# Optimization experiments

Hardware: AMD Instinct MI355X
Metric: run time of the kernel (lower is better)

Reference implementation:

```python
import jax, jax.numpy as jnp
import numpy as np

H = 256
NUM_REL = 480
NUM_ENT = 23000
N_TRIPLES = 8192
T = 10  # cur_ts == path_len window


def _lin_params(key, din, dout):
    kw, _ = jax.random.split(key)
    W = jax.random.normal(kw, (din, dout), dtype=jnp.float32) * 0.02
    b = jnp.zeros((dout,), dtype=jnp.float32)
    return W, b


def setup_inputs() -> dict:
    key = jax.random.key(0)
    ks = jax.random.split(key, 16)
    pre_emb = jax.random.normal(ks[0], (NUM_ENT, H), dtype=jnp.float32)
    r_emb = jax.random.normal(ks[1], (NUM_REL, H), dtype=jnp.float32)
    # history counts: sparse non-negative (zeros are masked to -1e9 in softmax)
    part = jax.random.uniform(ks[2], (N_TRIPLES, T * NUM_REL), dtype=jnp.float32)
    mask = jax.random.uniform(ks[3], (N_TRIPLES, T * NUM_REL)) < 0.3
    partial_embeding = jnp.where(mask, part, 0.0)
    sub_idx = jax.random.randint(ks[4], (N_TRIPLES,), 0, NUM_ENT)
    rel_idx = jax.random.randint(ks[5], (N_TRIPLES,), 0, NUM_REL)
    obj_idx = jax.random.randint(ks[6], (N_TRIPLES,), 0, NUM_ENT)
    Wm1, bm1 = _lin_params(ks[7], H, 2 * H)
    Wm2, bm2 = _lin_params(ks[8], 2 * H, H)
    Wattn, battn = _lin_params(ks[9], H, H)
    Wh1, bh1 = _lin_params(ks[10], H, H)
    Wh2, bh2 = _lin_params(ks[11], H, H)
    Walign, balign = _lin_params(ks[12], H, H)
    Wih = jax.random.normal(ks[13], (H, 3 * H), dtype=jnp.float32) * 0.02
    Whh = jax.random.normal(ks[14], (H, 3 * H), dtype=jnp.float32) * 0.02
    bih = jnp.zeros((3 * H,), dtype=jnp.float32)
    bhh = jnp.zeros((3 * H,), dtype=jnp.float32)
    return dict(pre_emb=pre_emb, r_emb=r_emb, partial_embeding=partial_embeding,
                sub_idx=sub_idx, rel_idx=rel_idx, obj_idx=obj_idx, cur_ts=T,
                Wm1=Wm1, bm1=bm1, Wm2=Wm2, bm2=bm2, Wattn=Wattn, battn=battn,
                Wh1=Wh1, bh1=bh1, Wh2=Wh2, bh2=bh2, Walign=Walign, balign=balign,
                Wih=Wih, Whh=Whh, bih=bih, bhh=bhh)


def _gru_cell(x, h, Wih, Whh, bih, bhh):
    # torch.nn.GRUCell math
    gi = x @ Wih + bih
    gh = h @ Whh + bhh
    i_r, i_z, i_n = jnp.split(gi, 3, axis=-1)
    h_r, h_z, h_n = jnp.split(gh, 3, axis=-1)
    r = jax.nn.sigmoid(i_r + h_r)
    z = jax.nn.sigmoid(i_z + h_z)
    n = jnp.tanh(i_n + r * h_n)
    return (1.0 - z) * n + z * h


def reference(pre_emb, r_emb, partial_embeding, sub_idx, rel_idx, obj_idx, cur_ts,
              Wm1, bm1, Wm2, bm2, Wattn, battn, Wh1, bh1, Wh2, bh2,
              Walign, balign, Wih, Whh, bih, bhh):
    n = partial_embeding.shape[0]
    num_rel = r_emb.shape[0]
    t = cur_ts  # path window covers [0, cur_ts)
    # relation mapping
    mapped_rel = (r_emb @ Wm1 + bm1) @ Wm2 + bm2            # [R, H]
    q_rel = mapped_rel[rel_idx]                               # [N, H]
    # attention logits base (loop-invariant): q W_attn mapped_rel^T
    base = (q_rel @ Wattn + battn) @ mapped_rel.T            # [N, R]
    # [N, t*R] -> [t, N, R] time-major slices
    hist = partial_embeding[:, : t * num_rel].reshape(n, t, num_rel).swapaxes(0, 1)
    h0 = jnp.zeros((n, mapped_rel.shape[1]), dtype=pre_emb.dtype)

    def step(h, cur):
        attn = cur * base
        attn = jax.nn.softmax(jnp.where(attn == 0, -1e9, attn), axis=1)
        x = attn @ mapped_rel                                 # [N, H]
        return _gru_cell(x, h, Wih, Whh, bih, bhh), None

    gru_hidden, _ = jax.lax.scan(step, h0, hist)
    # predicted history + match loss
    predicted_hist = 0.1 * ((q_rel @ Wh1 + bh1) @ Wh2 + bh2) + q_rel
    match_loss = jnp.mean((predicted_hist - gru_hidden) ** 2)
    # forward_forth (distmult)
    h2 = _gru_cell(q_rel, predicted_hist, Wih, Whh, bih, bhh)  # [N, H]
    sub = pre_emb[sub_idx]
    score_ = ((sub @ Walign + balign) * h2) @ (pre_emb @ Walign + balign).T  # [N, E]
    # BCE(sigmoid(score_), one_hot(obj)): per-elem -y*logsig(s) - (1-y)*logsig(-s)
    pos = score_[jnp.arange(n), obj_idx]
    path_loss = (-jnp.sum(jax.nn.log_sigmoid(-score_)) - jnp.sum(pos)) / (score_.size)
    score = jax.nn.sigmoid(score_)
    return match_loss, path_loss, score
```

## Files before the change

### kernel.cpp

```cpp
#include <hip/hip_runtime.h>
#include <hip/hip_bf16.h>
#include <stdint.h>

#define DEV __device__ __forceinline__

typedef unsigned short u16;
typedef __attribute__((ext_vector_type(8))) short bf16x8;
typedef __attribute__((ext_vector_type(4))) float f32x4;
typedef __attribute__((ext_vector_type(4))) unsigned short u16x4;

constexpr int H  = 256;
constexpr int R  = 480;
constexpr int RP = 512;
constexpr int NE = 23000;
constexpr int NT = 8192;
constexpr int TT = 10;

DEV u16 f2b(float f) {
  union { float f; unsigned u; } x; x.f = f;
  unsigned u = x.u;
  return (u16)((u + 0x7fffu + ((u >> 16) & 1u)) >> 16);
}
DEV float b2f(u16 h) {
  union { unsigned u; float f; } x; x.u = ((unsigned)h) << 16;
  return x.f;
}

DEV void gload_lds16(const u16* g, u16* lds) {
  __builtin_amdgcn_global_load_lds(
      (const __attribute__((address_space(1))) unsigned int*)g,
      (__attribute__((address_space(3))) unsigned int*)lds, 16, 0, 0);
}

__launch_bounds__(256)
__global__ void stageA_k(const float* __restrict__ r_emb,
                         const float* __restrict__ Wm1, const float* __restrict__ bm1,
                         const float* __restrict__ Wm2, const float* __restrict__ bm2,
                         const float* __restrict__ Wattn, const float* __restrict__ battn,
                         const float* __restrict__ Wih,
                         const float* __restrict__ Wh1, const float* __restrict__ bh1,
                         const float* __restrict__ Wh2, const float* __restrict__ bh2,
                         const float* __restrict__ Whh, const float* __restrict__ bhh,
                         const float* __restrict__ bih,
                         float* __restrict__ mapped, float* __restrict__ t1,
                         float* __restrict__ Pg, float* __restrict__ G2,
                         u16* __restrict__ MWT) {
  __shared__ float re[256], hid[512], mp[256], p1l[256], Pl[256];
  const int r = blockIdx.x, j = threadIdx.x;
  re[j] = r_emb[(size_t)r * 256 + j];
  __syncthreads();
  float s0 = bm1[j], s1 = bm1[j + 256];
  for (int k = 0; k < 256; ++k) {
    const float a = re[k];
    s0 += a * Wm1[(size_t)k * 512 + j];
    s1 += a * Wm1[(size_t)k * 512 + j + 256];
  }
  hid[j] = s0; hid[j + 256] = s1;
  __syncthreads();
  float m = bm2[j];
  for (int k = 0; k < 512; ++k) m += hid[k] * Wm2[(size_t)k * 256 + j];
  mp[j] = m; mapped[(size_t)r * 256 + j] = m;
  __syncthreads();
  float tv = battn[j];
  for (int k = 0; k < 256; ++k) tv += mp[k] * Wattn[(size_t)k * 256 + j];
  t1[(size_t)r * 256 + j] = tv;
  float mw0 = 0.f, mw1 = 0.f, mw2 = 0.f;
  for (int k = 0; k < 256; ++k) {
    const float a = mp[k];
    mw0 += a * Wih[(size_t)k * 768 + j];
    mw1 += a * Wih[(size_t)k * 768 + j + 256];
    mw2 += a * Wih[(size_t)k * 768 + j + 512];
  }
  MWT[(size_t)j * RP + r] = f2b(mw0);
  MWT[(size_t)(j + 256) * RP + r] = f2b(mw1);
  MWT[(size_t)(j + 512) * RP + r] = f2b(mw2);
  float pv = bh1[j];
  for (int k = 0; k < 256; ++k) pv += mp[k] * Wh1[(size_t)k * 256 + j];
  p1l[j] = pv;
  __syncthreads();
  float Pv = bh2[j];
  for (int k = 0; k < 256; ++k) Pv += p1l[k] * Wh2[(size_t)k * 256 + j];
  Pv = 0.1f * Pv + mp[j];
  Pl[j] = Pv; Pg[(size_t)r * 256 + j] = Pv;
  __syncthreads();
  float pw0 = bhh[j], pw1 = bhh[j + 256], pw2 = bhh[j + 512];
  for (int k = 0; k < 256; ++k) {
    const float a = Pl[k];
    pw0 += a * Whh[(size_t)k * 768 + j];
    pw1 += a * Whh[(size_t)k * 768 + j + 256];
    pw2 += a * Whh[(size_t)k * 768 + j + 512];
  }
  const float rg = 1.f / (1.f + __expf(-(mw0 + bih[j] + pw0)));
  const float zg = 1.f / (1.f + __expf(-(mw1 + bih[j + 256] + pw1)));
  const float ng = tanhf(mw2 + bih[j + 512] + rg * pw2);
  G2[(size_t)r * 256 + j] = (1.f - zg) * ng + zg * Pv;
}

__global__ void sgemm_bt_k(const float* __restrict__ A, const float* __restrict__ W,
                           float* __restrict__ C, int M, int N, int K) {
  const int idx = blockIdx.x * 256 + threadIdx.x;
  if (idx >= M * N) return;
  const int i = idx / N, j = idx % N;
  float s = 0.f;
  const float* a = A + (size_t)i * K;
  const float* w = W + (size_t)j * K;
  for (int k = 0; k < K; ++k) s += a[k] * w[k];
  C[idx] = s;
}

__global__ void prep_k(const float* __restrict__ Whh, const float* __restrict__ Walign,
                       const float* __restrict__ bih, const float* __restrict__ bhh,
                       u16* __restrict__ WhhT, u16* __restrict__ WalignT,
                       float* __restrict__ bsum) {
  const int b = blockIdx.x, tid = threadIdx.x;
  if (b < 768) {
    WhhT[(size_t)b * 256 + tid] = f2b(Whh[(size_t)tid * 768 + b]);
  } else if (b < 1024) {
    const int n = b - 768;
    WalignT[(size_t)n * 256 + tid] = f2b(Walign[(size_t)tid * 256 + n]);
  } else {
    const int c = (b - 1024) * 256 + tid;
    if (c < 768) bsum[c] = bih[c] + (c < 512 ? bhh[c] : 0.f);
  }
}

__global__ void softmax_all_k(const float* __restrict__ part, const float* __restrict__ B480,
                              const int* __restrict__ rel_idx, u16* __restrict__ attn) {
  const int task = blockIdx.x * 4 + (threadIdx.x >> 6);
  const int lane = threadIdx.x & 63;
  const int tt = task >> 13;
  const int i  = task & (NT - 1);
  const float* cur = part + (size_t)i * (TT * R) + (size_t)tt * R;
  const float* b = B480 + (size_t)rel_idx[i] * R;
  float v[8];
  float m = -3e38f;
  #pragma unroll
  for (int j = 0; j < 8; ++j) {
    const int r = lane + j * 64;
    float val = -1e9f;
    if (r < R) {
      const float c = cur[r];
      val = (c == 0.f) ? -1e9f : c * b[r];
      m = fmaxf(m, val);
    }
    v[j] = val;
  }
  #pragma unroll
  for (int o = 32; o; o >>= 1) m = fmaxf(m, __shfl_xor(m, o));
  float s = 0.f;
  #pragma unroll
  for (int j = 0; j < 8; ++j) {
    const int r = lane + j * 64;
    if (r < R) { v[j] = __expf(v[j] - m); s += v[j]; }
  }
  #pragma unroll
  for (int o = 32; o; o >>= 1) s += __shfl_xor(s, o);
  const float inv = 1.f / s;
  u16* arow = attn + (size_t)task * RP;
  #pragma unroll
  for (int j = 0; j < 8; ++j) {
    const int r = lane + j * 64;
    arow[r] = (r < R) ? f2b(v[j] * inv) : (u16)0;
  }
}

__launch_bounds__(256)
__global__ void scan_k(const u16* __restrict__ WhhT, const float* __restrict__ bhh,
                       const u16* __restrict__ gi_all, float* __restrict__ hbuf) {
  __shared__ __align__(16) u16 As[32 * 256];
  __shared__ __align__(16) u16 Bs[2][192 * 64];
  const int tid = threadIdx.x;
  const int lane = tid & 63;
  const int wv = tid >> 6;
  const int rf = wv >> 1;
  const int ch = wv & 1;
  const int fr = lane & 15;
  const int fq = lane >> 4;
  const int row_l = rf * 16 + fr;
  const int grow = blockIdx.x * 32 + row_l;
  const int sw = (fr & 7) * 8;

  auto stageB = [&](int buf, int cg, int k0) {
    #pragma unroll
    for (int it = 0; it < 6; ++it) {
      const int c = it * 256 + tid;
      const int vr = c >> 3, s = c & 7;
      const int vcol = ((vr >> 6) * 256) + cg * 64 + (vr & 63);
      gload_lds16(WhhT + (size_t)vcol * 256 + k0 + ((s ^ (vr & 7)) * 8),
                  &Bs[buf][(it * 256 + wv * 64) * 8]);
    }
  };

  float hreg[4][2][4];
  #pragma unroll
  for (int cg = 0; cg < 4; ++cg)
    #pragma unroll
    for (int nn = 0; nn < 2; ++nn)
      #pragma unroll
      for (int j = 0; j < 4; ++j) hreg[cg][nn][j] = 0.f;

  for (int t = 0; t < TT; ++t) {
    const u16* gi = gi_all + (size_t)t * NT * 768;
    #pragma unroll
    for (int cg = 0; cg < 4; ++cg) {
      f32x4 acc[6] = {};
      u16x4 gv[3][2];
      #pragma unroll
      for (int nn = 0; nn < 2; ++nn) {
        const int c = cg * 64 + ch * 32 + nn * 16 + fq * 4;
        const size_t gb = (size_t)grow * 768 + c;
        gv[0][nn] = *(const u16x4*)&gi[gb];
        gv[1][nn] = *(const u16x4*)&gi[gb + 256];
        gv[2][nn] = *(const u16x4*)&gi[gb + 512];
      }
      if (t > 0) {
        stageB(0, cg, 0);
        #pragma unroll
        for (int ki = 0; ki < 4; ++ki) {
          const int cb = ki & 1;
          if (ki < 3) {
            stageB(cb ^ 1, cg, (ki + 1) * 64);
            asm volatile("s_waitcnt vmcnt(6)" ::: "memory");
          } else {
            asm volatile("s_waitcnt vmcnt(0)" ::: "memory");
          }
          __builtin_amdgcn_sched_barrier(0);
          __builtin_amdgcn_s_barrier();
          #pragma unroll
          for (int kk = 0; kk < 2; ++kk) {
            const int ko = (ki * 64 + kk * 32 + fq * 8) ^ sw;
            const bf16x8 a = *(const bf16x8*)&As[row_l * 256 + ko];
            const int bo = (kk * 32 + fq * 8) ^ sw;
            #pragma unroll
            for (int g = 0; g < 3; ++g)
              #pragma unroll
              for (int nn = 0; nn < 2; ++nn) {
                const int vr = g * 64 + ch * 32 + nn * 16 + fr;
                const bf16x8 b = *(const bf16x8*)&Bs[cb][vr * 64 + bo];
                acc[g * 2 + nn] =
                    __builtin_amdgcn_mfma_f32_16x16x32_bf16(b, a, acc[g * 2 + nn], 0, 0, 0);
              }
          }
          __builtin_amdgcn_s_barrier();
        }
      }
      #pragma unroll
      for (int nn = 0; nn < 2; ++nn) {
        const int c = cg * 64 + ch * 32 + nn * 16 + fq * 4;
        const f32x4 bn = *(const f32x4*)&bhh[512 + c];
        #pragma unroll
        for (int j = 0; j < 4; ++j) {
          const float rg = 1.f / (1.f + __expf(-(b2f(gv[0][nn][j]) + acc[nn][j])));
          const float zg = 1.f / (1.f + __expf(-(b2f(gv[1][nn][j]) + acc[2 + nn][j])));
          const float ng = tanhf(b2f(gv[2][nn][j]) + rg * (acc[4 + nn][j] + bn[j]));
          hreg[cg][nn][j] = (1.f - zg) * ng + zg * hreg[cg][nn][j];
        }
      }
    }
    #pragma unroll
    for (int cg = 0; cg < 4; ++cg)
      #pragma unroll
      for (int nn = 0; nn < 2; ++nn) {
        const int c = cg * 64 + ch * 32 + nn * 16 + fq * 4;
        u16x4 o;
        #pragma unroll
        for (int j = 0; j < 4; ++j) o[j] = f2b(hreg[cg][nn][j]);
        *(u16x4*)&As[row_l * 256 + (c ^ sw)] = o;
        if (t == TT - 1) {
          f32x4 hv;
          #pragma unroll
          for (int j = 0; j < 4; ++j) hv[j] = hreg[cg][nn][j];
          *(f32x4*)&hbuf[(size_t)grow * 256 + c] = hv;
        }
      }
    __syncthreads();
  }
}

__global__ void gather_sub_k(const float* __restrict__ pre, const int* __restrict__ sub,
                             u16* __restrict__ sb) {
  const int q = blockIdx.x * 256 + threadIdx.x;
  const int i = q >> 6, c = (q & 63) * 4;
  const f32x4 v = *(const f32x4*)&pre[(size_t)sub[i] * H + c];
  u16x4 o;
  #pragma unroll
  for (int j = 0; j < 4; ++j) o[j] = f2b(v[j]);
  *(u16x4*)&sb[(size_t)q * 4] = o;
}
__global__ void cvt_pre_k(const float* __restrict__ pre, u16* __restrict__ pb) {
  const int q = blockIdx.x * 256 + threadIdx.x;
  const f32x4 v = *(const f32x4*)&pre[(size_t)q * 4];
  u16x4 o;
  #pragma unroll
  for (int j = 0; j < 4; ++j) o[j] = f2b(v[j]);
  *(u16x4*)&pb[(size_t)q * 4] = o;
}

__global__ void pos_k(const u16* __restrict__ lhs, const u16* __restrict__ alT,
                      const int* __restrict__ obj, float* __restrict__ pos) {
  const int row = blockIdx.x * 4 + (threadIdx.x >> 6);
  const int lane = threadIdx.x & 63;
  const u16x4 av = *(const u16x4*)&lhs[(size_t)row * H + lane * 4];
  const u16x4 bv = *(const u16x4*)&alT[(size_t)obj[row] * H + lane * 4];
  float s = 0.f;
  #pragma unroll
  for (int j = 0; j < 4; ++j) s += b2f(av[j]) * b2f(bv[j]);
  #pragma unroll
  for (int o = 32; o; o >>= 1) s += __shfl_down(s, o);
  if (lane == 0) pos[row] = s;
}

__global__ void finalize_k(const float* __restrict__ mp, const float* __restrict__ sp,
                           const float* __restrict__ pos, float* __restrict__ out) {
  const int tid = threadIdx.x;
  float s1 = 0.f, s2 = 0.f, s3 = 0.f;
  for (int i = tid; i < 128; i += 256) s1 += mp[i];
  for (int i = tid; i < 11520; i += 256) s2 += sp[i];
  for (int i = tid; i < 8192; i += 256) s3 += pos[i];
  #pragma unroll
  for (int o = 32; o; o >>= 1) {
    s1 += __shfl_down(s1, o); s2 += __shfl_down(s2, o); s3 += __shfl_down(s3, o);
  }
  __shared__ float r1[4], r2[4], r3[4];
  if ((tid & 63) == 0) { r1[tid >> 6] = s1; r2[tid >> 6] = s2; r3[tid >> 6] = s3; }
  __syncthreads();
  if (tid == 0) {
    const float a = r1[0] + r1[1] + r1[2] + r1[3];
    const float b = r2[0] + r2[1] + r2[2] + r2[3];
    const float c = r3[0] + r3[1] + r3[2] + r3[3];
    out[0] = a / 2097152.f;
    out[1] = (b - c) / 188416000.f;
  }
}

template <int MODE>
__launch_bounds__(256)
__global__ void gemm_k(const u16* __restrict__ A, const u16* __restrict__ Bt,
                       const float* __restrict__ bias,
                       float* __restrict__ Cf, u16* __restrict__ Cb,
                       int M, int N, int K,
                       float* __restrict__ out2, float* __restrict__ part,
                       const int* __restrict__ rel_idx, const float* __restrict__ Pf,
                       const float* __restrict__ G2f, const float* __restrict__ hf) {
  __shared__ __align__(16) u16 As[128 * 64];
  __shared__ __align__(16) u16 Bs[128 * 64];
  __shared__ float red[4];
  const int tid = threadIdx.x;
  const int lane = tid & 63;
  const int wv = tid >> 6;
  const int nbx = gridDim.x;
  int flat = blockIdx.y * nbx + blockIdx.x;
  const int nwg = nbx * gridDim.y;
  if ((nwg & 7) == 0) flat = (flat & 7) * (nwg >> 3) + (flat >> 3);
  const int bx = flat % nbx;
  const int by = flat / nbx;
  const int m0 = by * 128;
  const int n0 = bx * 128;
  const int wm = (wv >> 1) * 64;
  const int wn = (wv & 1) * 64;
  const int fr = lane & 15;
  const int fq = lane >> 4;
  const int sw = (lane & 7) * 8;
  f32x4 acc[4][4] = {};

  for (int k0 = 0; k0 < K; k0 += 64) {
    __syncthreads();
    #pragma unroll
    for (int it = 0; it < 4; ++it) {
      const int c = it * 256 + tid;
      const int row = c >> 3, s = c & 7;
      const int sc = (s ^ (row & 7)) * 8;
      int gr = m0 + row; gr = gr < M ? gr : M - 1;
      gload_lds16(A + (size_t)gr * K + k0 + sc, &As[(it * 256 + wv * 64) * 8]);
      int nr = n0 + row; nr = nr < N ? nr : N - 1;
      gload_lds16(Bt + (size_t)nr * K + k0 + sc, &Bs[(it * 256 + wv * 64) * 8]);
    }
    __syncthreads();
    #pragma unroll
    for (int kk = 0; kk < 2; ++kk) {
      const int ko = (kk * 32 + fq * 8) ^ sw;
      bf16x8 a[4], b[4];
      #pragma unroll
      for (int mi = 0; mi < 4; ++mi)
        a[mi] = *(const bf16x8*)&As[(wm + mi * 16 + fr) * 64 + ko];
      #pragma unroll
      for (int ni = 0; ni < 4; ++ni)
        b[ni] = *(const bf16x8*)&Bs[(wn + ni * 16 + fr) * 64 + ko];
      #pragma unroll
      for (int mi = 0; mi < 4; ++mi)
        #pragma unroll
        for (int ni = 0; ni < 4; ++ni)
          acc[mi][ni] = __builtin_amdgcn_mfma_f32_16x16x32_bf16(b[ni], a[mi], acc[mi][ni], 0, 0, 0);
    }
  }

  float local = 0.f;
  #pragma unroll
  for (int mi = 0; mi < 4; ++mi) {
    const int rowm = m0 + wm + mi * 16 + fr;
    int rel = 0;
    if (MODE == 2) rel = rel_idx[rowm];
    #pragma unroll
    for (int ni = 0; ni < 4; ++ni) {
      const int col = n0 + wn + ni * 16 + fq * 4;
      if (rowm < M && col < N) {
        f32x4 v = acc[mi][ni];
        if (MODE == 0) {
          if (bias != nullptr) {
            const f32x4 bv = *(const f32x4*)&bias[col];
            #pragma unroll
            for (int j = 0; j < 4; ++j) v[j] += bv[j];
          }
          if (Cf) *(f32x4*)&Cf[(size_t)rowm * N + col] = v;
          if (Cb) {
            u16x4 o;
            #pragma unroll
            for (int j = 0; j < 4; ++j) o[j] = f2b(v[j]);
            *(u16x4*)&Cb[(size_t)rowm * N + col] = o;
          }
        } else if (MODE == 1) {
          f32x4 sg;
          #pragma unroll
          for (int j = 0; j < 4; ++j) {
            const float s = v[j];
            const float sig = 1.f / (1.f + __expf(-s));
            sg[j] = sig;
            const float om = 1.f - sig;
            local += (om > 0.f) ? -__logf(om) : s;
          }
          *(f32x4*)&out2[(size_t)rowm * N + col] = sg;
        } else {
          const f32x4 bv = *(const f32x4*)&bias[col];
          const f32x4 Pv = *(const f32x4*)&Pf[(size_t)rel * H + col];
          const f32x4 Gv = *(const f32x4*)&G2f[(size_t)rel * H + col];
          const f32x4 hv = *(const f32x4*)&hf[(size_t)rowm * H + col];
          u16x4 o;
          #pragma unroll
          for (int j = 0; j < 4; ++j) {
            const float d = Pv[j] - hv[j];
            local += d * d;
            o[j] = f2b((v[j] + bv[j]) * Gv[j]);
          }
          *(u16x4*)&Cb[(size_t)rowm * N + col] = o;
        }
      }
    }
  }
  if (MODE != 0) {
    #pragma unroll
    for (int o = 32; o; o >>= 1) local += __shfl_down(local, o);
    if (lane == 0) red[wv] = local;
    __syncthreads();
    if (tid == 0) part[blockIdx.y * gridDim.x + blockIdx.x] = red[0] + red[1] + red[2] + red[3];
  }
}

extern "C" void kernel_launch(void* const* d_in, const int* in_sizes, int n_in,
                              void* d_out, int out_size, void* d_ws, size_t ws_size,
                              hipStream_t stream) {
  const float* pre_emb = (const float*)d_in[0];
  const float* r_emb   = (const float*)d_in[1];
  const float* part_e  = (const float*)d_in[2];
  const int*   sub_idx = (const int*)d_in[3];
  const int*   rel_idx = (const int*)d_in[4];
  const int*   obj_idx = (const int*)d_in[5];
  const float* Wm1 = (const float*)d_in[7];  const float* bm1 = (const float*)d_in[8];
  const float* Wm2 = (const float*)d_in[9];  const float* bm2 = (const float*)d_in[10];
  const float* Wattn = (const float*)d_in[11]; const float* battn = (const float*)d_in[12];
  const float* Wh1 = (const float*)d_in[13]; const float* bh1 = (const float*)d_in[14];
  const float* Wh2 = (const float*)d_in[15]; const float* bh2 = (const float*)d_in[16];
  const float* Walign = (const float*)d_in[17]; const float* balign = (const float*)d_in[18];
  const float* Wih = (const float*)d_in[19]; const float* Whh = (const float*)d_in[20];
  const float* bih = (const float*)d_in[21]; const float* bhh = (const float*)d_in[22];
  float* out = (float*)d_out;

  char* w = (char*)d_ws;
  size_t off = 0;
  auto alloc = [&](size_t bytes) -> void* {
    off = (off + 255) & ~(size_t)255;
    void* p = w + off;
    off += bytes;
    return p;
  };
  float* mapped = (float*)alloc((size_t)R * H * 4);
  float* t1     = (float*)alloc((size_t)R * H * 4);
  float* B480   = (float*)alloc((size_t)R * R * 4);
  float* P      = (float*)alloc((size_t)R * H * 4);
  float* G2     = (float*)alloc((size_t)R * H * 4);
  u16* MWT      = (u16*)alloc((size_t)768 * RP * 2);
  u16* WhhT     = (u16*)alloc((size_t)768 * H * 2);
  u16* WalignT  = (u16*)alloc((size_t)H * H * 2);
  float* bsum   = (float*)alloc(768 * 4);
  float* hbuf   = (float*)alloc((size_t)NT * H * 4);
  u16* lhs_b    = (u16*)alloc((size_t)NT * H * 2);
  u16* sub_b    = (u16*)alloc((size_t)NT * H * 2);
  u16* pre_b    = (u16*)alloc((size_t)NE * H * 2);
  u16* alT      = (u16*)alloc((size_t)NE * H * 2);
  float* mpart  = (float*)alloc(128 * 4);
  float* spart  = (float*)alloc(11520 * 4);
  float* posar  = (float*)alloc(8192 * 4);
  u16* attn_all = (u16*)alloc((size_t)TT * NT * RP * 2);
  u16* gi_all   = (u16*)alloc((size_t)TT * NT * 768 * 2);
  if (off > ws_size) return;

  hipMemsetAsync(MWT, 0, (size_t)768 * RP * 2, stream);
  stageA_k<<<R, 256, 0, stream>>>(r_emb, Wm1, bm1, Wm2, bm2, Wattn, battn, Wih,
                                  Wh1, bh1, Wh2, bh2, Whh, bhh, bih,
                                  mapped, t1, P, G2, MWT);
  sgemm_bt_k<<<(R * R + 255) / 256, 256, 0, stream>>>(t1, mapped, B480, R, R, H);
  prep_k<<<1027, 256, 0, stream>>>(Whh, Walign, bih, bhh, WhhT, WalignT, bsum);

  softmax_all_k<<<TT * (NT / 4), 256, 0, stream>>>(part_e, B480, rel_idx, attn_all);
  gemm_k<0><<<dim3(6, TT * (NT / 128)), 256, 0, stream>>>(
      attn_all, MWT, bsum, nullptr, gi_all, TT * NT, 768, RP,
      nullptr, nullptr, nullptr, nullptr, nullptr, nullptr);
  scan_k<<<NT / 32, 256, 0, stream>>>(WhhT, bhh, gi_all, hbuf);

  gather_sub_k<<<NT / 4, 256, 0, stream>>>(pre_emb, sub_idx, sub_b);
  gemm_k<2><<<dim3(2, 64), 256, 0, stream>>>(
      sub_b, WalignT, balign, nullptr, lhs_b, NT, H, H,
      nullptr, mpart, rel_idx, P, G2, hbuf);

  cvt_pre_k<<<NE / 4, 256, 0, stream>>>(pre_emb, pre_b);
  gemm_k<0><<<dim3(2, 180), 256, 0, stream>>>(
      pre_b, WalignT, balign, nullptr, alT, NE, H, H,
      nullptr, nullptr, nullptr, nullptr, nullptr, nullptr);

  gemm_k<1><<<dim3(180, 64), 256, 0, stream>>>(
      lhs_b, alT, nullptr, nullptr, nullptr, NT, NE, H,
      out + 2, spart, nullptr, nullptr, nullptr, nullptr);

  pos_k<<<2048, 256, 0, stream>>>(lhs_b, alT, obj_idx, posar);
  finalize_k<<<1, 256, 0, stream>>>(mpart, spart, posar, out);
}
```

Baseline: 1.109 ms.

## Double-buffer GEMM LDS tiles and fold weight prep into stageA kernel

The bf16 MFMA GEMM now uses two LDS buffers per operand, issuing the async global-to-LDS loads for the next K tile before computing on the current one and waiting with an explicit vmcnt. The goal is to overlap global memory latency with MFMA work. Separately, the weight transpose and bias-sum prep kernel is merged into stageA as extra blocks, removing one launch. Double buffering doubles LDS use per block (about 64KB), which can lower occupancy, and the hand-written waitcnt and barriers carry correctness risk.

```diff
diff --git a/kernel.cpp b/kernel.cpp
--- a/kernel.cpp
+++ b/kernel.cpp
@@ -41,12 +41,27 @@
                          const float* __restrict__ Wh1, const float* __restrict__ bh1,
                          const float* __restrict__ Wh2, const float* __restrict__ bh2,
                          const float* __restrict__ Whh, const float* __restrict__ bhh,
-                         const float* __restrict__ bih,
+                         const float* __restrict__ bih, const float* __restrict__ Walign,
                          float* __restrict__ mapped, float* __restrict__ t1,
                          float* __restrict__ Pg, float* __restrict__ G2,
-                         u16* __restrict__ MWT) {
+                         u16* __restrict__ MWT, u16* __restrict__ WhhT,
+                         u16* __restrict__ WalignT, float* __restrict__ bsum) {
   __shared__ float re[256], hid[512], mp[256], p1l[256], Pl[256];
-  const int r = blockIdx.x, j = threadIdx.x;
+  const int j = threadIdx.x;
+  if (blockIdx.x >= 480) {
+    const int b = blockIdx.x - 480;
+    if (b < 768) {
+      WhhT[(size_t)b * 256 + j] = f2b(Whh[(size_t)j * 768 + b]);
+    } else if (b < 1024) {
+      const int n = b - 768;
+      WalignT[(size_t)n * 256 + j] = f2b(Walign[(size_t)j * 256 + n]);
+    } else {
+      const int c = (b - 1024) * 256 + j;
+      if (c < 768) bsum[c] = bih[c] + (c < 512 ? bhh[c] : 0.f);
+    }
+    return;
+  }
+  const int r = blockIdx.x;
   re[j] = r_emb[(size_t)r * 256 + j];
   __syncthreads();
   float s0 = bm1[j], s1 = bm1[j + 256];
@@ -106,22 +121,6 @@
   const float* w = W + (size_t)j * K;
   for (int k = 0; k < K; ++k) s += a[k] * w[k];
   C[idx] = s;
-}
-
-__global__ void prep_k(const float* __restrict__ Whh, const float* __restrict__ Walign,
-                       const float* __restrict__ bih, const float* __restrict__ bhh,
-                       u16* __restrict__ WhhT, u16* __restrict__ WalignT,
-                       float* __restrict__ bsum) {
-  const int b = blockIdx.x, tid = threadIdx.x;
-  if (b < 768) {
-    WhhT[(size_t)b * 256 + tid] = f2b(Whh[(size_t)tid * 768 + b]);
-  } else if (b < 1024) {
-    const int n = b - 768;
-    WalignT[(size_t)n * 256 + tid] = f2b(Walign[(size_t)tid * 256 + n]);
-  } else {
-    const int c = (b - 1024) * 256 + tid;
-    if (c < 768) bsum[c] = bih[c] + (c < 512 ? bhh[c] : 0.f);
-  }
 }
 
 __global__ void softmax_all_k(const float* __restrict__ part, const float* __restrict__ B480,
@@ -342,8 +341,8 @@
                        float* __restrict__ out2, float* __restrict__ part,
                        const int* __restrict__ rel_idx, const float* __restrict__ Pf,
                        const float* __restrict__ G2f, const float* __restrict__ hf) {
-  __shared__ __align__(16) u16 As[128 * 64];
-  __shared__ __align__(16) u16 Bs[128 * 64];
+  __shared__ __align__(16) u16 As[2][128 * 64];
+  __shared__ __align__(16) u16 Bs[2][128 * 64];
   __shared__ float red[4];
   const int tid = threadIdx.x;
   const int lane = tid & 63;
@@ -363,35 +362,48 @@
   const int sw = (lane & 7) * 8;
   f32x4 acc[4][4] = {};
 
-  for (int k0 = 0; k0 < K; k0 += 64) {
-    __syncthreads();
+  auto stage = [&](int buf, int k0) {
     #pragma unroll
     for (int it = 0; it < 4; ++it) {
       const int c = it * 256 + tid;
       const int row = c >> 3, s = c & 7;
       const int sc = (s ^ (row & 7)) * 8;
       int gr = m0 + row; gr = gr < M ? gr : M - 1;
-      gload_lds16(A + (size_t)gr * K + k0 + sc, &As[(it * 256 + wv * 64) * 8]);
+      gload_lds16(A + (size_t)gr * K + k0 + sc, &As[buf][(it * 256 + wv * 64) * 8]);
       int nr = n0 + row; nr = nr < N ? nr : N - 1;
-      gload_lds16(Bt + (size_t)nr * K + k0 + sc, &Bs[(it * 256 + wv * 64) * 8]);
-    }
-    __syncthreads();
+      gload_lds16(Bt + (size_t)nr * K + k0 + sc, &Bs[buf][(it * 256 + wv * 64) * 8]);
+    }
+  };
+
+  stage(0, 0);
+  const int nsteps = K >> 6;
+  for (int kt = 0; kt < nsteps; ++kt) {
+    const int cb = kt & 1;
+    if (kt + 1 < nsteps) {
+      stage(cb ^ 1, (kt + 1) * 64);
+      asm volatile("s_waitcnt vmcnt(8)" ::: "memory");
+    } else {
+      asm volatile("s_waitcnt vmcnt(0)" ::: "memory");
+    }
+    __builtin_amdgcn_sched_barrier(0);
+    __builtin_amdgcn_s_barrier();
     #pragma unroll
     for (int kk = 0; kk < 2; ++kk) {
       const int ko = (kk * 32 + fq * 8) ^ sw;
       bf16x8 a[4], b[4];
       #pragma unroll
       for (int mi = 0; mi < 4; ++mi)
-        a[mi] = *(const bf16x8*)&As[(wm + mi * 16 + fr) * 64 + ko];
+        a[mi] = *(const bf16x8*)&As[cb][(wm + mi * 16 + fr) * 64 + ko];
       #pragma unroll
       for (int ni = 0; ni < 4; ++ni)
-        b[ni] = *(const bf16x8*)&Bs[(wn + ni * 16 + fr) * 64 + ko];
+        b[ni] = *(const bf16x8*)&Bs[cb][(wn + ni * 16 + fr) * 64 + ko];
       #pragma unroll
       for (int mi = 0; mi < 4; ++mi)
         #pragma unroll
         for (int ni = 0; ni < 4; ++ni)
           acc[mi][ni] = __builtin_amdgcn_mfma_f32_16x16x32_bf16(b[ni], a[mi], acc[mi][ni], 0, 0, 0);
     }
+    __builtin_amdgcn_s_barrier();
   }
 
   float local = 0.f;
@@ -504,11 +516,10 @@
   if (off > ws_size) return;
 
   hipMemsetAsync(MWT, 0, (size_t)768 * RP * 2, stream);
-  stageA_k<<<R, 256, 0, stream>>>(r_emb, Wm1, bm1, Wm2, bm2, Wattn, battn, Wih,
-                                  Wh1, bh1, Wh2, bh2, Whh, bhh, bih,
-                                  mapped, t1, P, G2, MWT);
+  stageA_k<<<480 + 1027, 256, 0, stream>>>(
+      r_emb, Wm1, bm1, Wm2, bm2, Wattn, battn, Wih, Wh1, bh1, Wh2, bh2,
+      Whh, bhh, bih, Walign, mapped, t1, P, G2, MWT, WhhT, WalignT, bsum);
   sgemm_bt_k<<<(R * R + 255) / 256, 256, 0, stream>>>(t1, mapped, B480, R, R, H);
-  prep_k<<<1027, 256, 0, stream>>>(Whh, Walign, bih, bhh, WhhT, WalignT, bsum);
 
   softmax_all_k<<<TT * (NT / 4), 256, 0, stream>>>(part_e, B480, rel_idx, attn_all);
   gemm_k<0><<<dim3(6, TT * (NT / 128)), 256, 0, stream>>>(
```

After: 1.094 ms. Within noise of the previous version (-1.4%).
